# Performance work log

Measured on AMD Instinct MI355X. Metric: run time of the kernel, lower is better.

Reference implementation:

```python
import jax, jax.numpy as jnp
import numpy as np

M = 512  # mem_dim

def silu(x):
    return x * jax.nn.sigmoid(x)

def layernorm(x, g, b, eps=1e-5):
    m = jnp.mean(x, axis=-1, keepdims=True)
    v = jnp.mean((x - m) ** 2, axis=-1, keepdims=True)
    return (x - m) * jax.lax.rsqrt(v + eps) * g + b

def dwconv(x, w, b):
    # x: [B,S,C], w: [C,1,K] depthwise, same padding
    y = jax.lax.conv_general_dilated(
        x.transpose(0, 2, 1), w, (1,), [(1, 1)],
        dimension_numbers=('NCH', 'OIH', 'NCH'), feature_group_count=x.shape[-1])
    return (y + b[None, :, None]).transpose(0, 2, 1)

def mlp(p, inp):
    W1, b1, W2, b2 = p
    return silu(inp @ W1.T + b1) @ W2.T + b2

def coeff(x, W1, b1, W2, b2):
    # x: [B,S,D] -> sigmoid scalar per token, averaged over batch -> [S]
    h = silu(jnp.einsum('bsd,hd->bsh', x, W1) + b1)
    c = jax.nn.sigmoid(jnp.einsum('bsh,oh->bso', h, W2) + b2)[..., 0]
    return jnp.mean(c, axis=0)

def setup_inputs() -> dict:
    key = jax.random.key(0)
    ks = jax.random.split(key, 24)
    B, S, D, H, CH, K = 8, 1024, 512, 32, 16, 3
    g = lambda k, shape, fan: jax.random.normal(k, shape, jnp.float32) / np.sqrt(fan)
    return {
        'x': jax.random.normal(ks[0], (B, S, D), jnp.float32),
        'Wk': g(ks[1], (M, D), D), 'Wv': g(ks[2], (M, D), D), 'Wq': g(ks[3], (M, D), D),
        'ck_w': g(ks[4], (M, 1, K), K), 'ck_b': g(ks[5], (M,), K),
        'cv_w': g(ks[6], (M, 1, K), K), 'cv_b': g(ks[7], (M,), K),
        'cq_w': g(ks[8], (M, 1, K), K), 'cq_b': g(ks[9], (M,), K),
        'ln_g': jnp.ones((M,), jnp.float32), 'ln_b': jnp.zeros((M,), jnp.float32),
        'W1': g(ks[10], (H, M), M), 'b1': jnp.zeros((H,), jnp.float32),
        'W2': g(ks[11], (M, H), H), 'b2': jnp.zeros((M,), jnp.float32),
        'aW1': g(ks[12], (CH, D), D), 'ab1': jnp.zeros((CH,), jnp.float32),
        'aW2': g(ks[13], (1, CH), CH), 'ab2': -2.0 * jnp.ones((1,), jnp.float32),
        'tW1': g(ks[14], (CH, D), D), 'tb1': jnp.zeros((CH,), jnp.float32),
        'tW2': g(ks[15], (1, CH), CH), 'tb2': -2.0 * jnp.ones((1,), jnp.float32),
        'eW1': g(ks[16], (CH, D), D), 'eb1': jnp.zeros((CH,), jnp.float32),
        'eW2': g(ks[17], (1, CH), CH), 'eb2': -2.0 * jnp.ones((1,), jnp.float32),
    }

def reference(x, Wk, Wv, Wq, ck_w, ck_b, cv_w, cv_b, cq_w, cq_b, ln_g, ln_b,
              W1, b1, W2, b2, aW1, ab1, aW2, ab2, tW1, tb1, tW2, tb2,
              eW1, eb1, eW2, eb2):
    k = layernorm(dwconv(x @ Wk.T, ck_w, ck_b), ln_g, ln_b)
    v = dwconv(x @ Wv.T, cv_w, cv_b)
    q = layernorm(dwconv(x @ Wq.T, cq_w, cq_b), ln_g, ln_b)
    alpha = coeff(x, aW1, ab1, aW2, ab2)  # [S]
    theta = coeff(x, tW1, tb1, tW2, tb2)
    eta = coeff(x, eW1, eb1, eW2, eb2)

    params0 = (W1, b1, W2, b2)
    S0 = jax.tree_util.tree_map(jnp.zeros_like, params0)

    def step(carry, xs_t):
        p, Sm = carry
        kt, vt, qt, a, th, e = xs_t  # kt/vt/qt: [B,M], a/th/e: scalar
        y = mlp(p, qt)  # output with pre-update params
        grad = jax.grad(lambda pp: jnp.mean((mlp(pp, kt) - vt) ** 2))(p)
        Sm = jax.tree_util.tree_map(lambda s, gi: e * s - th * gi, Sm, grad)
        p = jax.tree_util.tree_map(lambda pi, si: (1.0 - a) * pi + si, p, Sm)
        return (p, Sm), y

    xs = (k.transpose(1, 0, 2), v.transpose(1, 0, 2), q.transpose(1, 0, 2),
          alpha, theta, eta)
    _, ys = jax.lax.scan(step, (params0, S0), xs)
    return ys.transpose(1, 0, 2)  # [B,S,M]
```

## Files before the change

kernel.cpp:

```cpp
#include <hip/hip_runtime.h>
#include <hip/hip_bf16.h>
#include <cstdint>
#include <cstddef>

typedef __attribute__((ext_vector_type(8))) short bf16x8;
typedef __attribute__((ext_vector_type(4))) float f32x4;

#define DEV static __device__ __forceinline__

DEV float bf2f(uint16_t u){ union{uint32_t i; float f;} c; c.i = ((uint32_t)u) << 16; return c.f; }
DEV uint16_t f2bf(float f){ union{float f; uint32_t i;} c; c.f = f; uint32_t r = c.i + 0x7FFFu + ((c.i >> 16) & 1u); return (uint16_t)(r >> 16); }
DEV uint32_t cvtpk(float lo, float hi){
  uint32_t r;
  asm("v_cvt_pk_bf16_f32 %0, %1, %2" : "=v"(r) : "v"(lo), "v"(hi));
  return r;
}

DEV f32x4 mfma16(bf16x8 a, bf16x8 b, f32x4 c){
  return __builtin_amdgcn_mfma_f32_16x16x32_bf16(a, b, c, 0, 0, 0);
}

__global__ __launch_bounds__(128) void nltm_coeff(
    const float* __restrict__ x,
    const float* __restrict__ aW1, const float* __restrict__ ab1,
    const float* __restrict__ aW2, const float* __restrict__ ab2,
    const float* __restrict__ tW1, const float* __restrict__ tb1,
    const float* __restrict__ tW2, const float* __restrict__ tb2,
    const float* __restrict__ eW1, const float* __restrict__ eb1,
    const float* __restrict__ eW2, const float* __restrict__ eb2,
    float* __restrict__ gates)
{
  const int s = blockIdx.x, z = blockIdx.y;
  const int b = threadIdx.x >> 4, ch = threadIdx.x & 15;
  const float* w1 = (z==0)?aW1:(z==1)?tW1:eW1;
  const float* c1 = (z==0)?ab1:(z==1)?tb1:eb1;
  const float* w2 = (z==0)?aW2:(z==1)?tW2:eW2;
  const float* c2 = (z==0)?ab2:(z==1)?tb2:eb2;
  const float4* xp = (const float4*)(x + ((size_t)(b << 10) + s)*512);
  const float4* wp = (const float4*)(w1 + ch*512);
  float dot = 0.f;
  #pragma unroll 4
  for (int i = 0; i < 128; ++i){
    float4 a = xp[i], c = wp[i];
    dot += a.x*c.x + a.y*c.y + a.z*c.z + a.w*c.w;
  }
  dot += c1[ch];
  const float sg = 1.f / (1.f + __expf(-dot));
  float v = dot * sg * w2[ch];
  v += __shfl_xor(v, 1, 64);
  v += __shfl_xor(v, 2, 64);
  v += __shfl_xor(v, 4, 64);
  v += __shfl_xor(v, 8, 64);
  if (ch == 0){
    const float cc = 1.f / (1.f + __expf(-(v + c2[0])));
    atomicAdd(gates + (z << 10) + s, cc * 0.125f);
  }
}

__global__ __launch_bounds__(256) void nltm_gemm(
    const float* __restrict__ x, const float* __restrict__ Wk,
    const float* __restrict__ Wv, const float* __restrict__ Wq,
    uint16_t* __restrict__ preK, uint16_t* __restrict__ preV, uint16_t* __restrict__ preQ)
{
  __shared__ float As[16][132];
  __shared__ float Bs[16][132];
  const float* W = (blockIdx.z == 0) ? Wk : (blockIdx.z == 1) ? Wv : Wq;
  uint16_t* op  = (blockIdx.z == 0) ? preK : (blockIdx.z == 1) ? preV : preQ;
  const int tid = threadIdx.x;
  const int n0 = blockIdx.x << 7, m0 = blockIdx.y << 7;
  const int r = tid >> 1, cs = (tid & 1) << 3;
  const int ty = tid >> 4, tx = tid & 15;
  float acc[8][8];
  #pragma unroll
  for (int i = 0; i < 8; ++i)
    #pragma unroll
    for (int j = 0; j < 8; ++j) acc[i][j] = 0.f;

  for (int k0 = 0; k0 < 512; k0 += 16){
    float4 a0 = *(const float4*)(x + (size_t)(n0 + r)*512 + k0 + cs);
    float4 a1 = *(const float4*)(x + (size_t)(n0 + r)*512 + k0 + cs + 4);
    float4 b0 = *(const float4*)(W + (size_t)(m0 + r)*512 + k0 + cs);
    float4 b1 = *(const float4*)(W + (size_t)(m0 + r)*512 + k0 + cs + 4);
    __syncthreads();
    As[cs+0][r]=a0.x; As[cs+1][r]=a0.y; As[cs+2][r]=a0.z; As[cs+3][r]=a0.w;
    As[cs+4][r]=a1.x; As[cs+5][r]=a1.y; As[cs+6][r]=a1.z; As[cs+7][r]=a1.w;
    Bs[cs+0][r]=b0.x; Bs[cs+1][r]=b0.y; Bs[cs+2][r]=b0.z; Bs[cs+3][r]=b0.w;
    Bs[cs+4][r]=b1.x; Bs[cs+5][r]=b1.y; Bs[cs+6][r]=b1.z; Bs[cs+7][r]=b1.w;
    __syncthreads();
    #pragma unroll
    for (int kk = 0; kk < 16; ++kk){
      float4 av0 = *(const float4*)&As[kk][ty*8];
      float4 av1 = *(const float4*)&As[kk][ty*8+4];
      float4 bv0 = *(const float4*)&Bs[kk][tx*8];
      float4 bv1 = *(const float4*)&Bs[kk][tx*8+4];
      const float aa[8] = {av0.x,av0.y,av0.z,av0.w,av1.x,av1.y,av1.z,av1.w};
      const float bb[8] = {bv0.x,bv0.y,bv0.z,bv0.w,bv1.x,bv1.y,bv1.z,bv1.w};
      #pragma unroll
      for (int i = 0; i < 8; ++i)
        #pragma unroll
        for (int j = 0; j < 8; ++j)
          acc[i][j] = fmaf(aa[i], bb[j], acc[i][j]);
    }
  }
  #pragma unroll
  for (int i = 0; i < 8; ++i){
    const size_t n = (size_t)(n0 + ty*8 + i);
    uint4 v;
    v.x = (uint32_t)f2bf(acc[i][0]) | ((uint32_t)f2bf(acc[i][1]) << 16);
    v.y = (uint32_t)f2bf(acc[i][2]) | ((uint32_t)f2bf(acc[i][3]) << 16);
    v.z = (uint32_t)f2bf(acc[i][4]) | ((uint32_t)f2bf(acc[i][5]) << 16);
    v.w = (uint32_t)f2bf(acc[i][6]) | ((uint32_t)f2bf(acc[i][7]) << 16);
    *(uint4*)(op + n*512 + m0 + tx*8) = v;
  }
}

__global__ __launch_bounds__(512) void nltm_conv(
    const uint16_t* __restrict__ pre,
    const float* __restrict__ w, const float* __restrict__ wb,
    const float* __restrict__ lng, const float* __restrict__ lnb, const int doLN,
    uint16_t* __restrict__ post, uint16_t* __restrict__ postT)
{
  const int b = blockIdx.x >> 10, s = blockIdx.x & 1023;
  const int m = threadIdx.x;
  const size_t base = ((size_t)(b << 10) + s)*512 + m;
  const float xm = (s > 0)    ? bf2f(pre[base - 512]) : 0.f;
  const float x0 = bf2f(pre[base]);
  const float xp = (s < 1023) ? bf2f(pre[base + 512]) : 0.f;
  float y = fmaf(w[m*3], xm, fmaf(w[m*3+1], x0, fmaf(w[m*3+2], xp, wb[m])));
  if (doLN){
    __shared__ float red[2][8];
    float s1 = y, s2 = y*y;
    #pragma unroll
    for (int o = 32; o > 0; o >>= 1){
      s1 += __shfl_xor(s1, o, 64);
      s2 += __shfl_xor(s2, o, 64);
    }
    if ((threadIdx.x & 63) == 0){ red[0][threadIdx.x>>6] = s1; red[1][threadIdx.x>>6] = s2; }
    __syncthreads();
    float t1 = 0.f, t2 = 0.f;
    #pragma unroll
    for (int i = 0; i < 8; ++i){ t1 += red[0][i]; t2 += red[1][i]; }
    const float mean = t1 * (1.f/512.f);
    const float var  = t2 * (1.f/512.f) - mean*mean;
    y = (y - mean) * rsqrtf(var + 1e-5f) * lng[m] + lnb[m];
  }
  const uint16_t yb = f2bf(y);
  if (post)  post[((size_t)(s << 3) + b)*512 + m] = yb;
  if (postT) postT[(((size_t)s << 9) + m)*8 + b] = yb;
}

__global__ __launch_bounds__(1024) void nltm_scan(
    const float* __restrict__ W1g, const float* __restrict__ b1g,
    const float* __restrict__ W2g, const float* __restrict__ b2g,
    const float* __restrict__ gates,
    const uint16_t* __restrict__ kN, const uint16_t* __restrict__ qN,
    const uint16_t* __restrict__ kT, const uint16_t* __restrict__ vT,
    float* __restrict__ out)
{
  constexpr uint32_t W1Lo=0, W2No=33280, W2To=66048, QKLo=99328, VTo=115712,
                     KTo=123904, GOTo=132096, HQKo=140288, HKSTo=141312,
                     SILPo=141824, GPTo=143872, SCRo=144384, B1o=160768, B2o=160896;
  __shared__ __align__(16) char smem[162944];
  const int tid = threadIdx.x;
  const int lane = tid & 63;
  const int wid = tid >> 6;
  const int rb = lane & 15;
  const int kg = lane >> 4;

  float* b1L = (float*)(smem + B1o);
  float* b2L = (float*)(smem + B2o);

  float w1m[4][4], sm1[4][4], w2a[4][4], sma[4][4];
  #pragma unroll
  for (int i = 0; i < 4; ++i){
    const int tt = i >> 1, ht = i & 1;
    const int mA = (wid*2 + tt)*16;
    #pragma unroll
    for (int j = 0; j < 4; ++j){
      const int h1 = ht*16 + rb, m1 = mA + kg*4 + j;
      w1m[i][j] = W1g[h1*512 + m1];  sm1[i][j] = 0.f;
      w2a[i][j] = W2g[m1*32 + h1];   sma[i][j] = 0.f;
    }
  }
  float b2m = (tid < 512) ? b2g[tid] : 0.f, smb2 = 0.f;
  float b1m = (tid < 32) ? b1g[tid] : 0.f, smb1 = 0.f;

  for (int idx = tid; idx < 16384; idx += 1024){
    const int h = idx >> 9, m = idx & 511;
    *(uint16_t*)(smem + W1Lo + h*1040 + m*2) = f2bf(W1g[idx]);
    const int m2 = idx >> 5, h2 = idx & 31;
    const float w2v = W2g[idx];
    *(uint16_t*)(smem + W2No + m2*64 + (((h2>>3)^(m2&3))<<4) + ((h2&7)<<1)) = f2bf(w2v);
    *(uint16_t*)(smem + W2To + h2*1040 + m2*2) = f2bf(w2v);
  }
  if (tid < 32) b1L[tid] = b1g[tid];
  if (tid < 512) b2L[tid] = b2g[tid];

  {
    const int b = tid >> 7, m4 = (tid & 127) << 2;
    const uint32_t swz = (((m4>>3) ^ (b&7))<<4) + ((m4&7)<<1);
    *(uint2*)(smem + QKLo + b*1024 + swz)       = *(const uint2*)(qN + tid*4);
    *(uint2*)(smem + QKLo + (8+b)*1024 + swz)   = *(const uint2*)(kN + tid*4);
    if (tid < 512) *(uint4*)(smem + KTo + tid*16) = *(const uint4*)(kT + tid*8);
    else           *(uint4*)(smem + VTo + (tid-512)*16) = *(const uint4*)(vT + (tid-512)*8);
  }
  __syncthreads();

  const f32x4 cz = {0.f, 0.f, 0.f, 0.f};
  const bf16x8 zf = {0,0,0,0,0,0,0,0};
  const int ht_ = wid & 1, ks_ = wid >> 1;

  for (int t = 0; t < 1024; ++t){
    const int tn = (t < 1023) ? (t + 1) : 1023;
    uint2 pfq = *(const uint2*)(qN + (size_t)tn*4096 + tid*4);
    uint2 pfk = *(const uint2*)(kN + (size_t)tn*4096 + tid*4);
    uint4 pf4;
    if (lane < 32) pf4 = *(const uint4*)(kT + (size_t)tn*4096 + (wid*32 + lane)*8);
    else           pf4 = *(const uint4*)(vT + (size_t)tn*4096 + (wid*32 + lane - 32)*8);
    const float a_t = gates[t], th_t = gates[1024 + t], e_t = gates[2048 + t];
    const float oma = 1.f - a_t;

    {
      const uint32_t w1row = W1Lo + (uint32_t)(ht_*16 + rb)*1040;
      f32x4 acc = cz;
      #pragma unroll
      for (int u = 0; u < 2; ++u){
        const int c32 = ks_*2 + u;
        bf16x8 av = *(const bf16x8*)(smem + QKLo + rb*1024 + (((c32*4 + kg) ^ (rb&7)) << 4));
        bf16x8 bv = *(const bf16x8*)(smem + w1row + c32*64 + kg*16);
        acc = mfma16(av, bv, acc);
      }
      *(f32x4*)(smem + SCRo + ((wid*64 + lane) << 4)) = acc;
    }
    __syncthreads();

    if (wid < 2){
      const int ht = wid;
      f32x4 s = cz;
      #pragma unroll
      for (int ks = 0; ks < 8; ++ks)
        s += *(const f32x4*)(smem + SCRo + (((ks*2 + ht)*64 + lane) << 4));
      const int h = ht*16 + rb;
      const float b1v = b1L[h];
      float hs[4], sd[4];
      #pragma unroll
      for (int j = 0; j < 4; ++j){
        const float z = s[j] + b1v;
        const float sg = 1.f / (1.f + __expf(-z));
        hs[j] = z * sg;
        sd[j] = sg * (1.f + z * (1.f - sg));
      }
      #pragma unroll
      for (int j = 0; j < 4; ++j)
        *(uint16_t*)(smem + HQKo + (kg*4 + j)*64 + h*2) = f2bf(hs[j]);
      if (kg >= 2){
        uint2 hv; hv.x = cvtpk(hs[0], hs[1]); hv.y = cvtpk(hs[2], hs[3]);
        *(uint2*)(smem + HKSTo + h*16 + (kg-2)*8) = hv;
        f32x4 sv = {sd[0], sd[1], sd[2], sd[3]};
        *(f32x4*)(smem + SILPo + h*64 + (kg-2)*16) = sv;
      }
    }
    __syncthreads();

    {
      bf16x8 aF = *(const bf16x8*)(smem + HQKo + rb*64 + kg*16);
      #pragma unroll
      for (int u = 0; u < 2; ++u){
        const int mcol = (wid*2 + u)*16 + rb;
        bf16x8 bw = *(const bf16x8*)(smem + W2No + mcol*64 + ((kg ^ (mcol&3)) << 4));
        f32x4 c = mfma16(aF, bw, cz);
        const float b2v = b2L[mcol];
        if (kg < 2){
          #pragma unroll
          for (int j = 0; j < 4; ++j)
            out[(((size_t)(kg*4 + j) << 10) + t)*512 + mcol] = c[j] + b2v;
        } else {
          uint2 vt = *(const uint2*)(smem + VTo + mcol*16 + (kg-2)*8);
          float g0 = (c[0] + b2v - bf2f((uint16_t)vt.x))       * 4.8828125e-4f;
          float g1 = (c[1] + b2v - bf2f((uint16_t)(vt.x>>16))) * 4.8828125e-4f;
          float g2 = (c[2] + b2v - bf2f((uint16_t)vt.y))       * 4.8828125e-4f;
          float g3 = (c[3] + b2v - bf2f((uint16_t)(vt.y>>16))) * 4.8828125e-4f;
          uint2 gp; gp.x = cvtpk(g0, g1); gp.y = cvtpk(g2, g3);
          *(uint2*)(smem + GOTo + mcol*16 + (kg-2)*8) = gp;
          #pragma unroll
          for (int j = 0; j < 4; ++j){
            const int b = kg*4 + j - 8;
            const uint16_t gb = (uint16_t)((j & 1) ? ((j < 2 ? gp.x : gp.y) >> 16)
                                                   : (j < 2 ? gp.x : gp.y));
            *(uint16_t*)(smem + QKLo + (8+b)*1024 + (((mcol>>3) ^ (b&7)) << 4) + ((mcol&7) << 1)) = gb;
          }
        }
      }
    }
    __syncthreads();

    {
      const uint32_t w2row = W2To + (uint32_t)(ht_*16 + rb)*1040;
      f32x4 acc = cz;
      #pragma unroll
      for (int u = 0; u < 2; ++u){
        const int c32 = ks_*2 + u;
        bf16x8 av = (rb < 8) ? *(const bf16x8*)(smem + QKLo + (8+rb)*1024 + (((c32*4 + kg) ^ (rb&7)) << 4)) : zf;
        bf16x8 bv = *(const bf16x8*)(smem + w2row + c32*64 + kg*16);
        acc = mfma16(av, bv, acc);
      }
      *(f32x4*)(smem + SCRo + ((wid*64 + lane) << 4)) = acc;
    }
    __syncthreads();

    if (wid < 2 && kg < 2){
      const int ht = wid;
      f32x4 s = cz;
      #pragma unroll
      for (int ks = 0; ks < 8; ++ks)
        s += *(const f32x4*)(smem + SCRo + (((ks*2 + ht)*64 + lane) << 4));
      const int h = ht*16 + rb;
      f32x4 sp = *(const f32x4*)(smem + SILPo + h*64 + kg*16);
      uint2 w; w.x = cvtpk(s[0]*sp[0], s[1]*sp[1]); w.y = cvtpk(s[2]*sp[2], s[3]*sp[3]);
      *(uint2*)(smem + GPTo + h*16 + kg*8) = w;
    }
    __syncthreads();

    {
      bf16x8 hkF[2], gpF[2];
      #pragma unroll
      for (int ht = 0; ht < 2; ++ht){
        const int r0 = ht*16 + rb;
        hkF[ht] = (kg == 0) ? *(const bf16x8*)(smem + HKSTo + r0*16) : zf;
        gpF[ht] = (kg == 0) ? *(const bf16x8*)(smem + GPTo  + r0*16) : zf;
      }
      #pragma unroll
      for (int tt = 0; tt < 2; ++tt){
        const int mA = (wid*2 + tt)*16;
        bf16x8 ktf = (kg == 0) ? *(const bf16x8*)(smem + KTo  + (mA + rb)*16) : zf;
        bf16x8 gof = (kg == 0) ? *(const bf16x8*)(smem + GOTo + (mA + rb)*16) : zf;
        #pragma unroll
        for (int ht = 0; ht < 2; ++ht){
          const int i = tt*2 + ht;
          f32x4 g1 = mfma16(ktf, gpF[ht], cz);
          f32x4 g2 = mfma16(gof, hkF[ht], cz);
          #pragma unroll
          for (int j = 0; j < 4; ++j){
            sm1[i][j] = e_t*sm1[i][j] - th_t*g1[j];
            w1m[i][j] = oma*w1m[i][j] + sm1[i][j];
            sma[i][j] = e_t*sma[i][j] - th_t*g2[j];
            w2a[i][j] = oma*w2a[i][j] + sma[i][j];
          }
          uint2 u1; u1.x = cvtpk(w1m[i][0], w1m[i][1]); u1.y = cvtpk(w1m[i][2], w1m[i][3]);
          *(uint2*)(smem + W1Lo + (ht*16 + rb)*1040 + (mA + kg*4)*2) = u1;
          uint2 u2; u2.x = cvtpk(w2a[i][0], w2a[i][1]); u2.y = cvtpk(w2a[i][2], w2a[i][3]);
          *(uint2*)(smem + W2To + (ht*16 + rb)*1040 + (mA + kg*4)*2) = u2;
        }
      }
      #pragma unroll
      for (int tt = 0; tt < 2; ++tt){
        const int m2 = (wid*2 + tt)*16 + rb;
        #pragma unroll
        for (int ht = 0; ht < 2; ++ht){
          const uint32_t cb = W2To + (uint32_t)m2*2 + (uint32_t)(ht*16 + kg*4)*1040;
          uint16_t t0 = *(const uint16_t*)(smem + cb);
          uint16_t t1 = *(const uint16_t*)(smem + cb + 1040);
          uint16_t t2 = *(const uint16_t*)(smem + cb + 2080);
          uint16_t t3 = *(const uint16_t*)(smem + cb + 3120);
          uint2 u; u.x = (uint32_t)t0 | ((uint32_t)t1 << 16);
                   u.y = (uint32_t)t2 | ((uint32_t)t3 << 16);
          *(uint2*)(smem + W2No + m2*64 + ((((ht<<1)+(kg>>1)) ^ (m2&3)) << 4) + ((kg&1) << 3)) = u;
        }
      }
      if (tid < 512){
        uint4 gv = *(const uint4*)(smem + GOTo + tid*16);
        float gb2 = bf2f((uint16_t)gv.x) + bf2f((uint16_t)(gv.x>>16))
                  + bf2f((uint16_t)gv.y) + bf2f((uint16_t)(gv.y>>16))
                  + bf2f((uint16_t)gv.z) + bf2f((uint16_t)(gv.z>>16))
                  + bf2f((uint16_t)gv.w) + bf2f((uint16_t)(gv.w>>16));
        smb2 = e_t*smb2 - th_t*gb2;
        b2m = oma*b2m + smb2;
        b2L[tid] = b2m;
      }
      if (tid < 32){
        uint4 gv = *(const uint4*)(smem + GPTo + tid*16);
        float gb1 = bf2f((uint16_t)gv.x) + bf2f((uint16_t)(gv.x>>16))
                  + bf2f((uint16_t)gv.y) + bf2f((uint16_t)(gv.y>>16))
                  + bf2f((uint16_t)gv.z) + bf2f((uint16_t)(gv.z>>16))
                  + bf2f((uint16_t)gv.w) + bf2f((uint16_t)(gv.w>>16));
        smb1 = e_t*smb1 - th_t*gb1;
        b1m = oma*b1m + smb1;
        b1L[tid] = b1m;
      }
      {
        const int b = tid >> 7, m4 = (tid & 127) << 2;
        const uint32_t swz = (((m4>>3) ^ (b&7))<<4) + ((m4&7)<<1);
        *(uint2*)(smem + QKLo + b*1024 + swz)     = pfq;
        *(uint2*)(smem + QKLo + (8+b)*1024 + swz) = pfk;
        if (lane < 32) *(uint4*)(smem + KTo + (wid*32 + lane)*16)      = pf4;
        else           *(uint4*)(smem + VTo + (wid*32 + lane - 32)*16) = pf4;
      }
    }
    __syncthreads();
  }
}

extern "C" void kernel_launch(void* const* d_in, const int* in_sizes, int n_in,
                              void* d_out, int out_size, void* d_ws, size_t ws_size,
                              hipStream_t stream)
{
  const float* x   = (const float*)d_in[0];
  const float* Wk  = (const float*)d_in[1];
  const float* Wv  = (const float*)d_in[2];
  const float* Wq  = (const float*)d_in[3];
  const float* ckw = (const float*)d_in[4];
  const float* ckb = (const float*)d_in[5];
  const float* cvw = (const float*)d_in[6];
  const float* cvb = (const float*)d_in[7];
  const float* cqw = (const float*)d_in[8];
  const float* cqb = (const float*)d_in[9];
  const float* lng = (const float*)d_in[10];
  const float* lnb = (const float*)d_in[11];
  const float* W1g = (const float*)d_in[12];
  const float* b1g = (const float*)d_in[13];
  const float* W2g = (const float*)d_in[14];
  const float* b2g = (const float*)d_in[15];
  const float* aW1 = (const float*)d_in[16];
  const float* ab1 = (const float*)d_in[17];
  const float* aW2 = (const float*)d_in[18];
  const float* ab2 = (const float*)d_in[19];
  const float* tW1 = (const float*)d_in[20];
  const float* tb1 = (const float*)d_in[21];
  const float* tW2 = (const float*)d_in[22];
  const float* tb2 = (const float*)d_in[23];
  const float* eW1 = (const float*)d_in[24];
  const float* eb1 = (const float*)d_in[25];
  const float* eW2 = (const float*)d_in[26];
  const float* eb2 = (const float*)d_in[27];

  char* ws = (char*)d_ws;
  float* gates = (float*)ws;
  uint16_t* preK   = (uint16_t*)(ws + 16384);
  uint16_t* preV   = preK + 4194304;
  uint16_t* preQ   = preV + 4194304;
  uint16_t* postK  = preQ + 4194304;
  uint16_t* postQ  = postK + 4194304;
  uint16_t* postVT = postQ + 4194304;
  uint16_t* postKT = preV;

  hipMemsetAsync(gates, 0, 3*1024*sizeof(float), stream);
  nltm_coeff<<<dim3(1024,3), 128, 0, stream>>>(x, aW1,ab1,aW2,ab2, tW1,tb1,tW2,tb2,
                                               eW1,eb1,eW2,eb2, gates);
  nltm_gemm<<<dim3(64,4,3), 256, 0, stream>>>(x, Wk, Wv, Wq, preK, preV, preQ);
  nltm_conv<<<dim3(8192), 512, 0, stream>>>(preV, cvw, cvb, lng, lnb, 0, nullptr, postVT);
  nltm_conv<<<dim3(8192), 512, 0, stream>>>(preK, ckw, ckb, lng, lnb, 1, postK, postKT);
  nltm_conv<<<dim3(8192), 512, 0, stream>>>(preQ, cqw, cqb, lng, lnb, 1, postQ, nullptr);
  nltm_scan<<<dim3(1), dim3(1024), 0, stream>>>(W1g, b1g, W2g, b2g, gates,
                                                postK, postQ, postKT, postVT,
                                                (float*)d_out);
}
```

Before: 10.37 ms.

## Restructure single-block scan to 512 threads with fewer barriers and register-held W2 transpose

The sequential scan kernel drops from 1024 to 512 threads. Each wave now owns twice as many weight tiles, and the split-K reduction through shared scratch is gone: two waves compute the full W1·q and W2-side products with dual accumulators, which removes two barriers per timestep. A transposed copy of W2 and its momentum is kept in registers and updated by an extra MFMA, so the W2No layout is written directly instead of being rebuilt from W2To with scalar gathers. The cost is higher register pressure and more serial MFMA work on two waves, traded against fewer per-step synchronisations on the 1024-step serial critical path.

```diff
diff --git a/kernel.cpp b/kernel.cpp
--- a/kernel.cpp
+++ b/kernel.cpp
@@ -149,7 +149,7 @@
   if (postT) postT[(((size_t)s << 9) + m)*8 + b] = yb;
 }
 
-__global__ __launch_bounds__(1024) void nltm_scan(
+__global__ __launch_bounds__(512, 2) void nltm_scan(
     const float* __restrict__ W1g, const float* __restrict__ b1g,
     const float* __restrict__ W2g, const float* __restrict__ b2g,
     const float* __restrict__ gates,
@@ -159,8 +159,8 @@
 {
   constexpr uint32_t W1Lo=0, W2No=33280, W2To=66048, QKLo=99328, VTo=115712,
                      KTo=123904, GOTo=132096, HQKo=140288, HKSTo=141312,
-                     SILPo=141824, GPTo=143872, SCRo=144384, B1o=160768, B2o=160896;
-  __shared__ __align__(16) char smem[162944];
+                     SILPo=141824, GPTo=143872, B1o=144512, B2o=144640;
+  __shared__ __align__(16) char smem[146688];
   const int tid = threadIdx.x;
   const int lane = tid & 63;
   const int wid = tid >> 6;
@@ -170,22 +170,24 @@
   float* b1L = (float*)(smem + B1o);
   float* b2L = (float*)(smem + B2o);
 
-  float w1m[4][4], sm1[4][4], w2a[4][4], sma[4][4];
+  float w1m[8][4], sm1[8][4], w2a[8][4], sma[8][4], w2t[8][4], smt[8][4];
   #pragma unroll
-  for (int i = 0; i < 4; ++i){
+  for (int i = 0; i < 8; ++i){
     const int tt = i >> 1, ht = i & 1;
-    const int mA = (wid*2 + tt)*16;
+    const int mA = (wid*4 + tt)*16;
     #pragma unroll
     for (int j = 0; j < 4; ++j){
       const int h1 = ht*16 + rb, m1 = mA + kg*4 + j;
       w1m[i][j] = W1g[h1*512 + m1];  sm1[i][j] = 0.f;
       w2a[i][j] = W2g[m1*32 + h1];   sma[i][j] = 0.f;
-    }
-  }
-  float b2m = (tid < 512) ? b2g[tid] : 0.f, smb2 = 0.f;
+      const int h2 = ht*16 + kg*4 + j, m2 = mA + rb;
+      w2t[i][j] = W2g[m2*32 + h2];   smt[i][j] = 0.f;
+    }
+  }
+  float b2m = b2g[tid], smb2 = 0.f;
   float b1m = (tid < 32) ? b1g[tid] : 0.f, smb1 = 0.f;
 
-  for (int idx = tid; idx < 16384; idx += 1024){
+  for (int idx = tid; idx < 16384; idx += 512){
     const int h = idx >> 9, m = idx & 511;
     *(uint16_t*)(smem + W1Lo + h*1040 + m*2) = f2bf(W1g[idx]);
     const int m2 = idx >> 5, h2 = idx & 31;
@@ -194,58 +196,50 @@
     *(uint16_t*)(smem + W2To + h2*1040 + m2*2) = f2bf(w2v);
   }
   if (tid < 32) b1L[tid] = b1g[tid];
-  if (tid < 512) b2L[tid] = b2g[tid];
+  b2L[tid] = b2g[tid];
 
   {
-    const int b = tid >> 7, m4 = (tid & 127) << 2;
-    const uint32_t swz = (((m4>>3) ^ (b&7))<<4) + ((m4&7)<<1);
-    *(uint2*)(smem + QKLo + b*1024 + swz)       = *(const uint2*)(qN + tid*4);
-    *(uint2*)(smem + QKLo + (8+b)*1024 + swz)   = *(const uint2*)(kN + tid*4);
-    if (tid < 512) *(uint4*)(smem + KTo + tid*16) = *(const uint4*)(kT + tid*8);
-    else           *(uint4*)(smem + VTo + (tid-512)*16) = *(const uint4*)(vT + (tid-512)*8);
+    const int sb = tid >> 6, g64 = tid & 63;
+    const uint32_t swz = (uint32_t)((g64 ^ (sb & 7)) << 4);
+    *(uint4*)(smem + QKLo + sb*1024 + swz)       = *(const uint4*)(qN + tid*8);
+    *(uint4*)(smem + QKLo + (8+sb)*1024 + swz)   = *(const uint4*)(kN + tid*8);
+    *(uint4*)(smem + KTo + tid*16) = *(const uint4*)(kT + tid*8);
+    *(uint4*)(smem + VTo + tid*16) = *(const uint4*)(vT + tid*8);
   }
   __syncthreads();
 
   const f32x4 cz = {0.f, 0.f, 0.f, 0.f};
   const bf16x8 zf = {0,0,0,0,0,0,0,0};
-  const int ht_ = wid & 1, ks_ = wid >> 1;
 
   for (int t = 0; t < 1024; ++t){
     const int tn = (t < 1023) ? (t + 1) : 1023;
-    uint2 pfq = *(const uint2*)(qN + (size_t)tn*4096 + tid*4);
-    uint2 pfk = *(const uint2*)(kN + (size_t)tn*4096 + tid*4);
-    uint4 pf4;
-    if (lane < 32) pf4 = *(const uint4*)(kT + (size_t)tn*4096 + (wid*32 + lane)*8);
-    else           pf4 = *(const uint4*)(vT + (size_t)tn*4096 + (wid*32 + lane - 32)*8);
+    uint4 pfq  = *(const uint4*)(qN + (size_t)tn*4096 + tid*8);
+    uint4 pfk  = *(const uint4*)(kN + (size_t)tn*4096 + tid*8);
+    uint4 ktpf = *(const uint4*)(kT + (size_t)tn*4096 + tid*8);
+    uint4 vtpf = *(const uint4*)(vT + (size_t)tn*4096 + tid*8);
     const float a_t = gates[t], th_t = gates[1024 + t], e_t = gates[2048 + t];
     const float oma = 1.f - a_t;
 
-    {
-      const uint32_t w1row = W1Lo + (uint32_t)(ht_*16 + rb)*1040;
-      f32x4 acc = cz;
-      #pragma unroll
-      for (int u = 0; u < 2; ++u){
-        const int c32 = ks_*2 + u;
-        bf16x8 av = *(const bf16x8*)(smem + QKLo + rb*1024 + (((c32*4 + kg) ^ (rb&7)) << 4));
-        bf16x8 bv = *(const bf16x8*)(smem + w1row + c32*64 + kg*16);
-        acc = mfma16(av, bv, acc);
-      }
-      *(f32x4*)(smem + SCRo + ((wid*64 + lane) << 4)) = acc;
-    }
-    __syncthreads();
-
     if (wid < 2){
       const int ht = wid;
-      f32x4 s = cz;
-      #pragma unroll
-      for (int ks = 0; ks < 8; ++ks)
-        s += *(const f32x4*)(smem + SCRo + (((ks*2 + ht)*64 + lane) << 4));
+      const uint32_t w1row = W1Lo + (uint32_t)(ht*16 + rb)*1040;
+      f32x4 a0 = cz, a1 = cz;
+      #pragma unroll
+      for (int c = 0; c < 16; c += 2){
+        bf16x8 av0 = *(const bf16x8*)(smem + QKLo + rb*1024 + ((((c  )*4 + kg) ^ (rb&7)) << 4));
+        bf16x8 bv0 = *(const bf16x8*)(smem + w1row + c*64 + kg*16);
+        a0 = mfma16(av0, bv0, a0);
+        bf16x8 av1 = *(const bf16x8*)(smem + QKLo + rb*1024 + ((((c+1)*4 + kg) ^ (rb&7)) << 4));
+        bf16x8 bv1 = *(const bf16x8*)(smem + w1row + (c+1)*64 + kg*16);
+        a1 = mfma16(av1, bv1, a1);
+      }
+      f32x4 acc = a0 + a1;
       const int h = ht*16 + rb;
       const float b1v = b1L[h];
       float hs[4], sd[4];
       #pragma unroll
       for (int j = 0; j < 4; ++j){
-        const float z = s[j] + b1v;
+        const float z = acc[j] + b1v;
         const float sg = 1.f / (1.f + __expf(-z));
         hs[j] = z * sg;
         sd[j] = sg * (1.f + z * (1.f - sg));
@@ -265,8 +259,8 @@
     {
       bf16x8 aF = *(const bf16x8*)(smem + HQKo + rb*64 + kg*16);
       #pragma unroll
-      for (int u = 0; u < 2; ++u){
-        const int mcol = (wid*2 + u)*16 + rb;
+      for (int u = 0; u < 4; ++u){
+        const int mcol = (wid*4 + u)*16 + rb;
         bf16x8 bw = *(const bf16x8*)(smem + W2No + mcol*64 + ((kg ^ (mcol&3)) << 4));
         f32x4 c = mfma16(aF, bw, cz);
         const float b2v = b2L[mcol];
@@ -295,79 +289,76 @@
     __syncthreads();
 
     {
-      const uint32_t w2row = W2To + (uint32_t)(ht_*16 + rb)*1040;
-      f32x4 acc = cz;
-      #pragma unroll
-      for (int u = 0; u < 2; ++u){
-        const int c32 = ks_*2 + u;
-        bf16x8 av = (rb < 8) ? *(const bf16x8*)(smem + QKLo + (8+rb)*1024 + (((c32*4 + kg) ^ (rb&7)) << 4)) : zf;
-        bf16x8 bv = *(const bf16x8*)(smem + w2row + c32*64 + kg*16);
-        acc = mfma16(av, bv, acc);
-      }
-      *(f32x4*)(smem + SCRo + ((wid*64 + lane) << 4)) = acc;
-    }
-    __syncthreads();
-
-    if (wid < 2 && kg < 2){
-      const int ht = wid;
-      f32x4 s = cz;
-      #pragma unroll
-      for (int ks = 0; ks < 8; ++ks)
-        s += *(const f32x4*)(smem + SCRo + (((ks*2 + ht)*64 + lane) << 4));
-      const int h = ht*16 + rb;
-      f32x4 sp = *(const f32x4*)(smem + SILPo + h*64 + kg*16);
-      uint2 w; w.x = cvtpk(s[0]*sp[0], s[1]*sp[1]); w.y = cvtpk(s[2]*sp[2], s[3]*sp[3]);
-      *(uint2*)(smem + GPTo + h*16 + kg*8) = w;
-    }
-    __syncthreads();
-
-    {
-      bf16x8 hkF[2], gpF[2];
-      #pragma unroll
-      for (int ht = 0; ht < 2; ++ht){
-        const int r0 = ht*16 + rb;
-        hkF[ht] = (kg == 0) ? *(const bf16x8*)(smem + HKSTo + r0*16) : zf;
-        gpF[ht] = (kg == 0) ? *(const bf16x8*)(smem + GPTo  + r0*16) : zf;
-      }
-      #pragma unroll
-      for (int tt = 0; tt < 2; ++tt){
-        const int mA = (wid*2 + tt)*16;
-        bf16x8 ktf = (kg == 0) ? *(const bf16x8*)(smem + KTo  + (mA + rb)*16) : zf;
+      if (wid < 2){
+        const int ht = wid;
+        const uint32_t w2row = W2To + (uint32_t)(ht*16 + rb)*1040;
+        f32x4 a0 = cz, a1 = cz;
+        #pragma unroll
+        for (int c = 0; c < 16; c += 2){
+          bf16x8 av0 = (rb < 8) ? *(const bf16x8*)(smem + QKLo + (8+rb)*1024 + ((((c  )*4 + kg) ^ (rb&7)) << 4)) : zf;
+          bf16x8 bv0 = *(const bf16x8*)(smem + w2row + c*64 + kg*16);
+          a0 = mfma16(av0, bv0, a0);
+          bf16x8 av1 = (rb < 8) ? *(const bf16x8*)(smem + QKLo + (8+rb)*1024 + ((((c+1)*4 + kg) ^ (rb&7)) << 4)) : zf;
+          bf16x8 bv1 = *(const bf16x8*)(smem + w2row + (c+1)*64 + kg*16);
+          a1 = mfma16(av1, bv1, a1);
+        }
+        f32x4 acc = a0 + a1;
+        if (kg < 2){
+          const int h = ht*16 + rb;
+          f32x4 sp = *(const f32x4*)(smem + SILPo + h*64 + kg*16);
+          uint2 w; w.x = cvtpk(acc[0]*sp[0], acc[1]*sp[1]);
+                   w.y = cvtpk(acc[2]*sp[2], acc[3]*sp[3]);
+          *(uint2*)(smem + GPTo + h*16 + kg*8) = w;
+        }
+      }
+      bf16x8 hkF0 = (kg == 0) ? *(const bf16x8*)(smem + HKSTo + rb*16)        : zf;
+      bf16x8 hkF1 = (kg == 0) ? *(const bf16x8*)(smem + HKSTo + (16+rb)*16)   : zf;
+      #pragma unroll
+      for (int tt = 0; tt < 4; ++tt){
+        const int mA = (wid*4 + tt)*16;
         bf16x8 gof = (kg == 0) ? *(const bf16x8*)(smem + GOTo + (mA + rb)*16) : zf;
         #pragma unroll
         for (int ht = 0; ht < 2; ++ht){
           const int i = tt*2 + ht;
-          f32x4 g1 = mfma16(ktf, gpF[ht], cz);
-          f32x4 g2 = mfma16(gof, hkF[ht], cz);
+          f32x4 g2  = mfma16(gof, ht ? hkF1 : hkF0, cz);
+          f32x4 g2t = mfma16(ht ? hkF1 : hkF0, gof, cz);
+          #pragma unroll
+          for (int j = 0; j < 4; ++j){
+            sma[i][j] = e_t*sma[i][j] - th_t*g2[j];
+            w2a[i][j] = oma*w2a[i][j] + sma[i][j];
+            smt[i][j] = e_t*smt[i][j] - th_t*g2t[j];
+            w2t[i][j] = oma*w2t[i][j] + smt[i][j];
+          }
+        }
+      }
+    }
+    __syncthreads();
+
+    {
+      bf16x8 gpF0 = (kg == 0) ? *(const bf16x8*)(smem + GPTo + rb*16)      : zf;
+      bf16x8 gpF1 = (kg == 0) ? *(const bf16x8*)(smem + GPTo + (16+rb)*16) : zf;
+      #pragma unroll
+      for (int tt = 0; tt < 4; ++tt){
+        const int mA = (wid*4 + tt)*16;
+        bf16x8 ktf = (kg == 0) ? *(const bf16x8*)(smem + KTo + (mA + rb)*16) : zf;
+        #pragma unroll
+        for (int ht = 0; ht < 2; ++ht){
+          const int i = tt*2 + ht;
+          f32x4 g1 = mfma16(ktf, ht ? gpF1 : gpF0, cz);
           #pragma unroll
           for (int j = 0; j < 4; ++j){
             sm1[i][j] = e_t*sm1[i][j] - th_t*g1[j];
             w1m[i][j] = oma*w1m[i][j] + sm1[i][j];
-            sma[i][j] = e_t*sma[i][j] - th_t*g2[j];
-            w2a[i][j] = oma*w2a[i][j] + sma[i][j];
           }
           uint2 u1; u1.x = cvtpk(w1m[i][0], w1m[i][1]); u1.y = cvtpk(w1m[i][2], w1m[i][3]);
           *(uint2*)(smem + W1Lo + (ht*16 + rb)*1040 + (mA + kg*4)*2) = u1;
           uint2 u2; u2.x = cvtpk(w2a[i][0], w2a[i][1]); u2.y = cvtpk(w2a[i][2], w2a[i][3]);
           *(uint2*)(smem + W2To + (ht*16 + rb)*1040 + (mA + kg*4)*2) = u2;
+          uint2 u3; u3.x = cvtpk(w2t[i][0], w2t[i][1]); u3.y = cvtpk(w2t[i][2], w2t[i][3]);
+          *(uint2*)(smem + W2No + (mA + rb)*64 + ((((ht<<1)+(kg>>1)) ^ (rb&3)) << 4) + ((kg&1) << 3)) = u3;
         }
       }
-      #pragma unroll
-      for (int tt = 0; tt < 2; ++tt){
-        const int m2 = (wid*2 + tt)*16 + rb;
-        #pragma unroll
-        for (int ht = 0; ht < 2; ++ht){
-          const uint32_t cb = W2To + (uint32_t)m2*2 + (uint32_t)(ht*16 + kg*4)*1040;
-          uint16_t t0 = *(const uint16_t*)(smem + cb);
-          uint16_t t1 = *(const uint16_t*)(smem + cb + 1040);
-          uint16_t t2 = *(const uint16_t*)(smem + cb + 2080);
-          uint16_t t3 = *(const uint16_t*)(smem + cb + 3120);
-          uint2 u; u.x = (uint32_t)t0 | ((uint32_t)t1 << 16);
-                   u.y = (uint32_t)t2 | ((uint32_t)t3 << 16);
-          *(uint2*)(smem + W2No + m2*64 + ((((ht<<1)+(kg>>1)) ^ (m2&3)) << 4) + ((kg&1) << 3)) = u;
-        }
-      }
-      if (tid < 512){
+      {
         uint4 gv = *(const uint4*)(smem + GOTo + tid*16);
         float gb2 = bf2f((uint16_t)gv.x) + bf2f((uint16_t)(gv.x>>16))
                   + bf2f((uint16_t)gv.y) + bf2f((uint16_t)(gv.y>>16))
@@ -388,12 +379,12 @@
         b1L[tid] = b1m;
       }
       {
-        const int b = tid >> 7, m4 = (tid & 127) << 2;
-        const uint32_t swz = (((m4>>3) ^ (b&7))<<4) + ((m4&7)<<1);
-        *(uint2*)(smem + QKLo + b*1024 + swz)     = pfq;
-        *(uint2*)(smem + QKLo + (8+b)*1024 + swz) = pfk;
-        if (lane < 32) *(uint4*)(smem + KTo + (wid*32 + lane)*16)      = pf4;
-        else           *(uint4*)(smem + VTo + (wid*32 + lane - 32)*16) = pf4;
+        const int sb = tid >> 6, g64 = tid & 63;
+        const uint32_t swz = (uint32_t)((g64 ^ (sb & 7)) << 4);
+        *(uint4*)(smem + QKLo + sb*1024 + swz)     = pfq;
+        *(uint4*)(smem + QKLo + (8+sb)*1024 + swz) = pfk;
+        *(uint4*)(smem + KTo + tid*16) = ktpf;
+        *(uint4*)(smem + VTo + tid*16) = vtpf;
       }
     }
     __syncthreads();
@@ -450,7 +441,7 @@
   nltm_conv<<<dim3(8192), 512, 0, stream>>>(preV, cvw, cvb, lng, lnb, 0, nullptr, postVT);
   nltm_conv<<<dim3(8192), 512, 0, stream>>>(preK, ckw, ckb, lng, lnb, 1, postK, postKT);
   nltm_conv<<<dim3(8192), 512, 0, stream>>>(preQ, cqw, cqb, lng, lnb, 1, postQ, nullptr);
-  nltm_scan<<<dim3(1), dim3(1024), 0, stream>>>(W1g, b1g, W2g, b2g, gates,
-                                                postK, postQ, postKT, postVT,
-                                                (float*)d_out);
-}
+  nltm_scan<<<dim3(1), dim3(512), 0, stream>>>(W1g, b1g, W2g, b2g, gates,
+                                               postK, postQ, postKT, postVT,
+                                               (float*)d_out);
+}
```

New measurement: 18.21 ms. +75.5%, slower.
